# Optimization experiments

Hardware: AMD Instinct MI355X
Metric: run time of the kernel (lower is better)

The kernel has to match this reference:

```python
import jax, jax.numpy as jnp
import numpy as np

OUT, IN = 4096, 4096
PACKED = (OUT * IN + 1) // 2


def setup_inputs() -> dict:
    key = jax.random.key(0)
    k1, k2, k3, k4, k5 = jax.random.split(key, 5)
    x = jax.random.normal(k1, (4, 2048, IN), dtype=jnp.float32)
    weight_packed = jax.random.randint(k2, (PACKED,), 0, 256, dtype=jnp.int32)
    scale = jax.random.uniform(k3, (OUT, 1), dtype=jnp.float32) * 0.01 + 1e-4
    zero_point = jax.random.uniform(k4, (OUT, 1), dtype=jnp.float32) * 8.0
    bias = jax.random.normal(k5, (OUT,), dtype=jnp.float32) * 0.02
    return {"x": x, "weight_packed": weight_packed, "scale": scale,
            "zero_point": zero_point, "bias": bias}


def _dequant_weight(weight_packed, scale, zero_point):
    # Unpack two 4-bit nibbles per byte; low nibble first (matches torch.stack dim=1 + flatten)
    low = (weight_packed & 15).astype(jnp.float32)          # [PACKED]
    high = ((weight_packed >> 4) & 15).astype(jnp.float32)   # [PACKED]
    unpacked = jnp.stack([low, high], axis=1).reshape(-1)     # [2*PACKED]
    w = unpacked[: OUT * IN].reshape(OUT, IN)
    # weight * scale - zero_point * scale == (weight - zero_point) * scale
    return (w - zero_point) * scale                           # [OUT, IN]


def reference(x, weight_packed, scale, zero_point, bias):
    w = _dequant_weight(weight_packed, scale, zero_point)
    # F.linear: x @ w.T + bias
    return jnp.einsum('bsi,oi->bso', x, w) + bias
```

## Files before the change

kernel.cpp:

```cpp
#include <hip/hip_runtime.h>
#include <hip/hip_bf16.h>


typedef __bf16 bf16;
typedef __attribute__((ext_vector_type(8))) __bf16 bf16x8;
typedef __attribute__((ext_vector_type(4))) float f32x4;
typedef __attribute__((ext_vector_type(4))) unsigned int u32x4;

#define OUT_DIM 4096
#define IN_DIM  4096
#define M_DIM   8192

__global__ __launch_bounds__(256) void cvt_x_kernel(
    const float* __restrict__ x, bf16* __restrict__ xb, float* __restrict__ rowsum)
{
  const long t = (long)blockIdx.x * 256 + threadIdx.x;
  const long i = t * 8;
  const f32x4 a = *(const f32x4*)(x + i);
  const f32x4 b = *(const f32x4*)(x + i + 4);
  union { bf16 h[8]; u32x4 u; } r;
#pragma unroll
  for (int q = 0; q < 4; ++q) { r.h[q] = (bf16)a[q]; r.h[4+q] = (bf16)b[q]; }
  *(u32x4*)(xb + i) = r.u;
  float p = 0.f;
#pragma unroll
  for (int q = 0; q < 8; ++q) p += (float)r.h[q];
#pragma unroll
  for (int off = 32; off > 0; off >>= 1) p += __shfl_down(p, off);
  if ((threadIdx.x & 63) == 0) atomicAdd(&rowsum[(long)(t >> 9)], p);
}

__global__ __launch_bounds__(256) void repack_w_kernel(
    const int* __restrict__ wp, unsigned int* __restrict__ wb)
{
  const long t = (long)blockIdx.x * 256 + threadIdx.x;
  const long e = t * 16;
  u32x4 r;
#pragma unroll
  for (int q = 0; q < 4; ++q) {
    const int4 p = *(const int4*)(wp + e + q * 4);
    r[q] = (unsigned)(p.x & 255) | ((unsigned)(p.y & 255) << 8) |
           ((unsigned)(p.z & 255) << 16) | ((unsigned)(p.w & 255) << 24);
  }
  *(u32x4*)(wb + t * 4) = r;
}

__global__ __launch_bounds__(512, 2) void gemm_bt_bias_kernel(
    const bf16* __restrict__ A, const unsigned char* __restrict__ WP,
    const float* __restrict__ scale, const float* __restrict__ zp,
    const float* __restrict__ bias, const float* __restrict__ rowsum,
    float* __restrict__ C)
{
  const int N = OUT_DIM, K = IN_DIM;
  const int NT = IN_DIM / 64;

  __shared__ bf16 smA[2][2][256][32];
  __shared__ unsigned int smB[2][2][1024];

  const int bid = blockIdx.x;
  const int swz = (bid & 7) * (512 / 8) + (bid >> 3);
  const int bm = swz >> 4;
  const int bn = swz & 15;

  const int tid  = threadIdx.x;
  const int lane = tid & 63;
  const int wave = tid >> 6;
  const int wr = wave >> 2;
  const int wc = wave & 3;

  const long row0 = (long)bm * 256;
  const long col0 = (long)bn * 256;

  const int L0 = tid * 16;
  const int L1 = 8192 + tid * 16;
  const int Lw0 = L0 ^ (((L0 >> 9) & 1) << 5);
  const int Lw1 = L1 ^ (((L1 >> 9) & 1) << 5);
  const int sr0 = Lw0 >> 6, sc0 = (Lw0 & 63) >> 1;
  const int sr1 = Lw1 >> 6, sc1 = (Lw1 & 63) >> 1;
  const bf16* a0 = A + (row0 + sr0) * (long)K + sc0;
  const bf16* a1 = A + (row0 + sr1) * (long)K + sc1;

  const int W0 = tid, W1 = 512 + tid;
  const long bn0 = col0 + (W0 >> 8) * 64 + (W0 & 3) * 16 + ((W0 >> 4) & 15);
  const long bn1 = col0 + (W1 >> 8) * 64 + (W1 & 3) * 16 + ((W1 >> 4) & 15);
  const unsigned char* w0 = WP + bn0 * 2048L + ((W0 >> 2) & 3) * 4;
  const unsigned char* w1 = WP + bn1 * 2048L + ((W1 >> 2) & 3) * 4;

#define STAGE_G(BUF, KS, KOFF) do {                                             \
    char* Ah = (char*)&smA[BUF][KS][0][0];                                      \
    char* Bh = (char*)&smB[BUF][KS][0];                                         \
    __builtin_amdgcn_global_load_lds(                                           \
        (const __attribute__((address_space(1))) void*)(a0 + (KOFF)),           \
        (__attribute__((address_space(3))) void*)(Ah + L0), 16, 0, 0);          \
    __builtin_amdgcn_global_load_lds(                                           \
        (const __attribute__((address_space(1))) void*)(a1 + (KOFF)),           \
        (__attribute__((address_space(3))) void*)(Ah + L1), 16, 0, 0);          \
    __builtin_amdgcn_global_load_lds(                                           \
        (const __attribute__((address_space(1))) void*)(w0 + ((KOFF) >> 1)),    \
        (__attribute__((address_space(3))) void*)(Bh + tid * 4), 4, 0, 0);      \
    __builtin_amdgcn_global_load_lds(                                           \
        (const __attribute__((address_space(1))) void*)(w1 + ((KOFF) >> 1)),    \
        (__attribute__((address_space(3))) void*)(Bh + 2048 + tid * 4), 4, 0, 0);\
  } while (0)

  const int lane15 = lane & 15;
  const int rb  = (lane15 * 64 + ((lane >> 4) << 4)) ^ ((lane & 8) << 2);
  const int wrB = wr * 8192;
  const int rBb = ((wc * 16 + lane15) * 4 + (lane >> 4)) * 16;

  float sv16[4], ev[4];
#pragma unroll
  for (int f = 0; f < 4; ++f) {
    const int n = (int)col0 + wc * 64 + f * 16 + lane15;
    const float s = scale[n];
    sv16[f] = 16.f * s;
    ev[f]   = s * (16.f + zp[n]);
  }

  f32x4 acc[8][4] = {};

#define PHASE(BUF, KS, STAGE_STMT, VM_STMT) do {                                \
    VM_STMT;                                                                    \
    __builtin_amdgcn_s_barrier();                                               \
    asm volatile("" ::: "memory");        \
    const char* Ab = (const char*)&smA[BUF][KS][0][0];                          \
    const char* Bp = (const char*)&smB[BUF][KS][0];                             \
    const u32x4 pkv = *(const u32x4*)(Bp + rBb);                                \
    bf16x8 fa[8];                                                               \
    _Pragma("unroll")                                                           \
    for (int f = 0; f < 8; ++f) fa[f] = *(const bf16x8*)(Ab + wrB + f * 1024 + rb); \
    STAGE_STMT;                                                                 \
    bf16x8 fb[4];                                                               \
    _Pragma("unroll")                                                           \
    for (int f = 0; f < 4; ++f) {                                               \
      union { unsigned int u[4]; bf16x8 h; } bb;                                \
      const unsigned int pk = pkv[f];                                           \
      _Pragma("unroll")                                                         \
      for (int g = 0; g < 4; ++g) {                                             \
        const unsigned int tt = pk >> (8 * g);                                  \
        bb.u[g] = 0x3F803F80u | ((tt & 15u) << 3) | ((tt & 0xF0u) << 15);       \
      }                                                                         \
      fb[f] = bb.h;                                                             \
    }                                                                           \
    __builtin_amdgcn_s_setprio(1);                                              \
    _Pragma("unroll")                                                           \
    for (int i = 0; i < 8; ++i)                                                 \
      _Pragma("unroll")                                                         \
      for (int j = 0; j < 4; ++j)                                               \
        acc[i][j] = __builtin_amdgcn_mfma_f32_16x16x32_bf16(fa[i], fb[j], acc[i][j], 0, 0, 0); \
    __builtin_amdgcn_s_setprio(0);                                              \
  } while (0)

  STAGE_G(0, 0, 0);
  STAGE_G(0, 1, 32);

  for (int T = 0; T < NT; ++T) {
    const int buf = T & 1;
    const int nbuf = buf ^ 1;
    const int nko = (T + 1) * 64;
    const bool st = (T + 1 < NT);

    PHASE(buf, 0,
          { if (st) STAGE_G(nbuf, 0, nko); },
          { asm volatile("s_waitcnt vmcnt(4)" ::: "memory"); });
    PHASE(buf, 1,
          { if (st) STAGE_G(nbuf, 1, nko + 32); },
          { if (T == NT - 1) asm volatile("s_waitcnt vmcnt(0)" ::: "memory");
            else             asm volatile("s_waitcnt vmcnt(4)" ::: "memory"); });
  }

  const long cr0 = row0 + wr * 128 + ((lane >> 4) << 2);
  const long cc0 = col0 + wc * 64 + lane15;
#pragma unroll
  for (int j = 0; j < 4; ++j) {
    const long gc = cc0 + j * 16;
    const float bv = bias[gc];
    const float sj = sv16[j], e = ev[j];
#pragma unroll
    for (int mf = 0; mf < 8; ++mf) {
      const long gr = cr0 + mf * 16;
      float* cp = C + gr * (long)N + gc;
#pragma unroll
      for (int r = 0; r < 4; ++r)
        cp[(long)r * N] = acc[mf][j][r] * sj - e * rowsum[gr + r] + bv;
    }
  }
#undef PHASE
#undef STAGE_G
}

extern "C" void kernel_launch(void* const* d_in, const int* in_sizes, int n_in,
                              void* d_out, int out_size, void* d_ws, size_t ws_size,
                              hipStream_t stream)
{
  const float* x     = (const float*)d_in[0];
  const int*   wp    = (const int*)d_in[1];
  const float* scale = (const float*)d_in[2];
  const float* zp    = (const float*)d_in[3];
  const float* bias  = (const float*)d_in[4];
  float* out = (float*)d_out;

  bf16* Xb = (bf16*)d_ws;
  unsigned int* Wb = (unsigned int*)((char*)d_ws + 67108864);
  float* Rs = (float*)((char*)d_ws + 67108864 + 8388608);

  hipMemsetAsync(Rs, 0, M_DIM * sizeof(float), stream);
  cvt_x_kernel<<<(M_DIM * (long)IN_DIM / 8) / 256, 256, 0, stream>>>(x, Xb, Rs);
  repack_w_kernel<<<(OUT_DIM * (long)IN_DIM / 2 / 16) / 256, 256, 0, stream>>>(wp, Wb);
  gemm_bt_bias_kernel<<<512, 512, 0, stream>>>(
      Xb, (const unsigned char*)Wb, scale, zp, bias, Rs, out);
}
```

Before: 310.7 us.

## Shrink GEMM block tile to 256x128 with four waves and more blocks

Changes the GEMM block tile from 256x256 with 8 waves to 256x128 with 4 waves, doubling the grid to 1024 blocks. Each thread now issues four A loads per stage, the B LDS buffer is halved, and the vmcnt waits are adjusted to match. The aim is better occupancy and load balance across CUs, with smaller LDS per block. The cost is that every A tile is loaded twice as often, so global traffic for A rises, and the remapping of the PHASE code (not shown) must still be consistent with the 2x2 wave layout.

```diff
diff --git a/kernel.cpp b/kernel.cpp
--- a/kernel.cpp
+++ b/kernel.cpp
@@ -45,7 +45,7 @@
   *(u32x4*)(wb + t * 4) = r;
 }
 
-__global__ __launch_bounds__(512, 2) void gemm_bt_bias_kernel(
+__global__ __launch_bounds__(256, 2) void gemm_bt_bias_kernel(
     const bf16* __restrict__ A, const unsigned char* __restrict__ WP,
     const float* __restrict__ scale, const float* __restrict__ zp,
     const float* __restrict__ bias, const float* __restrict__ rowsum,
@@ -55,32 +55,33 @@
   const int NT = IN_DIM / 64;
 
   __shared__ bf16 smA[2][2][256][32];
-  __shared__ unsigned int smB[2][2][1024];
+  __shared__ unsigned int smB[2][2][512];
 
   const int bid = blockIdx.x;
-  const int swz = (bid & 7) * (512 / 8) + (bid >> 3);
-  const int bm = swz >> 4;
-  const int bn = swz & 15;
+  const int swz = (bid & 7) * 128 + (bid >> 3);
+  const int bm = swz >> 5;
+  const int bn = swz & 31;
 
   const int tid  = threadIdx.x;
   const int lane = tid & 63;
   const int wave = tid >> 6;
-  const int wr = wave >> 2;
-  const int wc = wave & 3;
+  const int wr = wave >> 1;
+  const int wc = wave & 1;
 
   const long row0 = (long)bm * 256;
-  const long col0 = (long)bn * 256;
-
-  const int L0 = tid * 16;
-  const int L1 = 8192 + tid * 16;
-  const int Lw0 = L0 ^ (((L0 >> 9) & 1) << 5);
-  const int Lw1 = L1 ^ (((L1 >> 9) & 1) << 5);
-  const int sr0 = Lw0 >> 6, sc0 = (Lw0 & 63) >> 1;
-  const int sr1 = Lw1 >> 6, sc1 = (Lw1 & 63) >> 1;
-  const bf16* a0 = A + (row0 + sr0) * (long)K + sc0;
-  const bf16* a1 = A + (row0 + sr1) * (long)K + sc1;
-
-  const int W0 = tid, W1 = 512 + tid;
+  const long col0 = (long)bn * 128;
+
+  const bf16* aP0; const bf16* aP1; const bf16* aP2; const bf16* aP3;
+  {
+#define MKA(c, P) { const int L = (c)*4096 + tid*16;                            \
+      const int Lw = L ^ (((L >> 9) & 1) << 5);                                 \
+      P = A + (row0 + (Lw >> 6)) * (long)K + ((Lw & 63) >> 1); }
+    MKA(0, aP0) MKA(1, aP1) MKA(2, aP2) MKA(3, aP3)
+#undef MKA
+  }
+  const int LA = tid * 16;
+
+  const int W0 = tid, W1 = 256 + tid;
   const long bn0 = col0 + (W0 >> 8) * 64 + (W0 & 3) * 16 + ((W0 >> 4) & 15);
   const long bn1 = col0 + (W1 >> 8) * 64 + (W1 & 3) * 16 + ((W1 >> 4) & 15);
   const unsigned char* w0 = WP + bn0 * 2048L + ((W0 >> 2) & 3) * 4;
@@ -90,17 +91,23 @@
     char* Ah = (char*)&smA[BUF][KS][0][0];                                      \
     char* Bh = (char*)&smB[BUF][KS][0];                                         \
     __builtin_amdgcn_global_load_lds(                                           \
-        (const __attribute__((address_space(1))) void*)(a0 + (KOFF)),           \
-        (__attribute__((address_space(3))) void*)(Ah + L0), 16, 0, 0);          \
-    __builtin_amdgcn_global_load_lds(                                           \
-        (const __attribute__((address_space(1))) void*)(a1 + (KOFF)),           \
-        (__attribute__((address_space(3))) void*)(Ah + L1), 16, 0, 0);          \
+        (const __attribute__((address_space(1))) void*)(aP0 + (KOFF)),          \
+        (__attribute__((address_space(3))) void*)(Ah + LA), 16, 0, 0);          \
+    __builtin_amdgcn_global_load_lds(                                           \
+        (const __attribute__((address_space(1))) void*)(aP1 + (KOFF)),          \
+        (__attribute__((address_space(3))) void*)(Ah + 4096 + LA), 16, 0, 0);   \
+    __builtin_amdgcn_global_load_lds(                                           \
+        (const __attribute__((address_space(1))) void*)(aP2 + (KOFF)),          \
+        (__attribute__((address_space(3))) void*)(Ah + 8192 + LA), 16, 0, 0);   \
+    __builtin_amdgcn_global_load_lds(                                           \
+        (const __attribute__((address_space(1))) void*)(aP3 + (KOFF)),          \
+        (__attribute__((address_space(3))) void*)(Ah + 12288 + LA), 16, 0, 0);  \
     __builtin_amdgcn_global_load_lds(                                           \
         (const __attribute__((address_space(1))) void*)(w0 + ((KOFF) >> 1)),    \
         (__attribute__((address_space(3))) void*)(Bh + tid * 4), 4, 0, 0);      \
     __builtin_amdgcn_global_load_lds(                                           \
         (const __attribute__((address_space(1))) void*)(w1 + ((KOFF) >> 1)),    \
-        (__attribute__((address_space(3))) void*)(Bh + 2048 + tid * 4), 4, 0, 0);\
+        (__attribute__((address_space(3))) void*)(Bh + 1024 + tid * 4), 4, 0, 0);\
   } while (0)
 
   const int lane15 = lane & 15;
@@ -162,11 +169,11 @@
 
     PHASE(buf, 0,
           { if (st) STAGE_G(nbuf, 0, nko); },
-          { asm volatile("s_waitcnt vmcnt(4)" ::: "memory"); });
+          { asm volatile("s_waitcnt vmcnt(6)" ::: "memory"); });
     PHASE(buf, 1,
           { if (st) STAGE_G(nbuf, 1, nko + 32); },
           { if (T == NT - 1) asm volatile("s_waitcnt vmcnt(0)" ::: "memory");
-            else             asm volatile("s_waitcnt vmcnt(4)" ::: "memory"); });
+            else             asm volatile("s_waitcnt vmcnt(6)" ::: "memory"); });
   }
 
   const long cr0 = row0 + wr * 128 + ((lane >> 4) << 2);
@@ -207,6 +214,6 @@
   hipMemsetAsync(Rs, 0, M_DIM * sizeof(float), stream);
   cvt_x_kernel<<<(M_DIM * (long)IN_DIM / 8) / 256, 256, 0, stream>>>(x, Xb, Rs);
   repack_w_kernel<<<(OUT_DIM * (long)IN_DIM / 2 / 16) / 256, 256, 0, stream>>>(wp, Wb);
-  gemm_bt_bias_kernel<<<512, 512, 0, stream>>>(
+  gemm_bt_bias_kernel<<<1024, 256, 0, stream>>>(
       Xb, (const unsigned char*)Wb, scale, zp, bias, Rs, out);
 }
```

After: 311.1 us. About the same (+0.1%).
